# Performance work log

Hardware: AMD Instinct MI355X
Metric: run time of the kernel (lower is better)

Reference implementation:

```python
import jax, jax.numpy as jnp
import numpy as np
from jax.ops import segment_sum

N_NODES = 100000

def gcn_conv(x, ei, W, b, n):
    # PyG GCNConv: add self-loops, symmetric deg^-1/2 normalization,
    # linear transform (no lin bias), scatter-sum at target, then conv bias.
    src = jnp.concatenate([ei[0], jnp.arange(n)])  # [E+N]
    dst = jnp.concatenate([ei[1], jnp.arange(n)])
    deg = segment_sum(jnp.ones_like(dst, dtype=x.dtype), dst, num_segments=n)
    dinv = jnp.where(deg > 0, jax.lax.rsqrt(deg), 0.0)
    norm = dinv[src] * dinv[dst]                   # [E+N]
    h = x @ W.T                                    # [N, out] transform before gather
    msg = h[src] * norm[:, None]                   # [E+N, out]
    return segment_sum(msg, dst, num_segments=n) + b

def sage_conv_mean(x, ei, Wl, bl, Wr, n):
    # PyG SAGEConv(aggr='mean'): out = lin_l(mean_{j->i} x_j) + lin_r(x_i)
    src, dst = ei[0], ei[1]
    s = segment_sum(x[src], dst, num_segments=n)   # [N, d]
    cnt = segment_sum(jnp.ones_like(dst, dtype=x.dtype), dst, num_segments=n)
    mean = s / jnp.maximum(cnt, 1.0)[:, None]
    return mean @ Wl.T + bl + x @ Wr.T

def setup_inputs() -> dict:
    key = jax.random.key(0)
    k1, k2, k3, k4, k5, k6 = jax.random.split(key, 6)
    in_dim, hid = 128, 128
    n, e = N_NODES, 1600000
    feat = jax.random.normal(k1, (n, in_dim), dtype=jnp.float32)
    ei = jax.random.randint(k2, (2, e), 0, n, dtype=jnp.int64)
    W1 = jax.random.normal(k3, (hid, in_dim), dtype=jnp.float32) * 0.05
    b1 = jnp.zeros((hid,), dtype=jnp.float32)
    Wl = jax.random.normal(k4, (hid, hid), dtype=jnp.float32) * 0.05
    bl = jnp.zeros((hid,), dtype=jnp.float32)
    Wr = jax.random.normal(k5, (hid, hid), dtype=jnp.float32) * 0.05
    return {"feat": feat, "ei": ei, "W1": W1, "b1": b1, "Wl": Wl, "bl": bl, "Wr": Wr}

def reference(feat, ei, W1, b1, Wl, bl, Wr):
    n = feat.shape[0]
    h = jax.nn.relu(gcn_conv(feat, ei, W1, b1, n))
    h = jax.nn.relu(sage_conv_mean(h, ei, Wl, bl, Wr, n))
    return h
```

## Files before the change

### kernel.cpp

```cpp
#include <hip/hip_runtime.h>

typedef unsigned int uint;
typedef unsigned short ushort;
typedef short sv8 __attribute__((ext_vector_type(8)));
typedef float f32x4 __attribute__((ext_vector_type(4)));
typedef ushort u16x8 __attribute__((ext_vector_type(8)));

__device__ __forceinline__ ushort f2b(float f) {
  uint u = __float_as_uint(f);
  return (ushort)((u + 0x7FFFu + ((u >> 16) & 1u)) >> 16);
}
__device__ __forceinline__ float b2f_lo(uint p) { return __uint_as_float(p << 16); }
__device__ __forceinline__ float b2f_hi(uint p) { return __uint_as_float(p & 0xFFFF0000u); }
__device__ __forceinline__ uint cvtpk(float lo, float hi) {
  uint r;
  asm("v_cvt_pk_bf16_f32 %0, %1, %2" : "=v"(r) : "v"(lo), "v"(hi));
  return r;
}

#define MFMA16(acc, a, b) \
  asm volatile("v_mfma_f32_16x16x32_bf16 %0, %1, %2, %0" : "+v"(acc) : "v"(a), "v"(b))
#define DOT2(acc, p, d) \
  asm("v_dot2_f32_bf16 %0, %1, %2, %0" : "+v"(acc) : "v"(p), "v"(d))

#define GATHER16(SRC, jj)                                                     \
  {                                                                           \
    uint pa = (uint)__shfl((int)packed, (jj) + q);                            \
    uint pb = (uint)__shfl((int)packed, (jj) + 4 + q);                        \
    uint pc = (uint)__shfl((int)packed, (jj) + 8 + q);                        \
    uint pd = (uint)__shfl((int)packed, (jj) + 12 + q);                       \
    uint4 va = *(const uint4*)&SRC[(size_t)(pa & 0x1FFFFu) * 128 + lc * 8];   \
    uint4 vb = *(const uint4*)&SRC[(size_t)(pb & 0x1FFFFu) * 128 + lc * 8];   \
    uint4 vc = *(const uint4*)&SRC[(size_t)(pc & 0x1FFFFu) * 128 + lc * 8];   \
    uint4 vd = *(const uint4*)&SRC[(size_t)(pd & 0x1FFFFu) * 128 + lc * 8];   \
    uint dab = (pa >> 17) | ((pb >> 17) << 16);                               \
    uint dcd = (pc >> 17) | ((pd >> 17) << 16);                               \
    uint p;                                                                   \
    p = __builtin_amdgcn_perm(va.x, vb.x, 0x01000504u); DOT2(acc[0], p, dab); \
    p = __builtin_amdgcn_perm(va.x, vb.x, 0x03020706u); DOT2(acc[1], p, dab); \
    p = __builtin_amdgcn_perm(va.y, vb.y, 0x01000504u); DOT2(acc[2], p, dab); \
    p = __builtin_amdgcn_perm(va.y, vb.y, 0x03020706u); DOT2(acc[3], p, dab); \
    p = __builtin_amdgcn_perm(va.z, vb.z, 0x01000504u); DOT2(acc[4], p, dab); \
    p = __builtin_amdgcn_perm(va.z, vb.z, 0x03020706u); DOT2(acc[5], p, dab); \
    p = __builtin_amdgcn_perm(va.w, vb.w, 0x01000504u); DOT2(acc[6], p, dab); \
    p = __builtin_amdgcn_perm(va.w, vb.w, 0x03020706u); DOT2(acc[7], p, dab); \
    p = __builtin_amdgcn_perm(vc.x, vd.x, 0x01000504u); DOT2(acc[0], p, dcd); \
    p = __builtin_amdgcn_perm(vc.x, vd.x, 0x03020706u); DOT2(acc[1], p, dcd); \
    p = __builtin_amdgcn_perm(vc.y, vd.y, 0x01000504u); DOT2(acc[2], p, dcd); \
    p = __builtin_amdgcn_perm(vc.y, vd.y, 0x03020706u); DOT2(acc[3], p, dcd); \
    p = __builtin_amdgcn_perm(vc.z, vd.z, 0x01000504u); DOT2(acc[4], p, dcd); \
    p = __builtin_amdgcn_perm(vc.z, vd.z, 0x03020706u); DOT2(acc[5], p, dcd); \
    p = __builtin_amdgcn_perm(vc.w, vd.w, 0x01000504u); DOT2(acc[6], p, dcd); \
    p = __builtin_amdgcn_perm(vc.w, vd.w, 0x03020706u); DOT2(acc[7], p, dcd); \
  }


__global__ __launch_bounds__(256) void k_bhist(const int* __restrict__ dst,
                                               int* __restrict__ bhist, int E) {
  __shared__ int h[256];
  int t = threadIdx.x;
  h[t] = 0;
  __syncthreads();
#pragma unroll
  for (int i = 0; i < 16; ++i) {
    int idx = blockIdx.x * 16384 + i * 1024 + t * 4;
    if (idx + 4 <= E) {
      int4 d = *(const int4*)&dst[idx];
      atomicAdd(&h[d.x >> 10], 1);
      atomicAdd(&h[d.y >> 10], 1);
      atomicAdd(&h[d.z >> 10], 1);
      atomicAdd(&h[d.w >> 10], 1);
    } else {
      for (int k = 0; k < 4; ++k)
        if (idx + k < E) atomicAdd(&h[dst[idx + k] >> 10], 1);
    }
  }
  __syncthreads();
  if (h[t] > 0) atomicAdd(&bhist[t], h[t]);
}

__global__ __launch_bounds__(256) void k_bscan(const int* __restrict__ bhist,
                                               int* __restrict__ bbase,
                                               int* __restrict__ bcursor,
                                               int* __restrict__ rowptr,
                                               int NB, int N, int E) {
  __shared__ int s[256];
  int t = threadIdx.x;
  int v = (t < NB) ? bhist[t] : 0;
  s[t] = v;
  __syncthreads();
  for (int off = 1; off < 256; off <<= 1) {
    int u = (t >= off) ? s[t - off] : 0;
    __syncthreads();
    s[t] += u;
    __syncthreads();
  }
  if (t < NB) {
    bbase[t] = s[t] - v;
    bcursor[t] = s[t] - v;
  }
  if (t == 0) rowptr[N] = E;
}

__global__ __launch_bounds__(256) void k_scatter(const int* __restrict__ ei,
                                                 int* __restrict__ bcursor,
                                                 uint* __restrict__ keyval, int E) {
  __shared__ int h[256];
  __shared__ int base[256];
  int t = threadIdx.x;
  h[t] = 0;
  __syncthreads();
#pragma unroll
  for (int i = 0; i < 16; ++i) {
    int idx = blockIdx.x * 16384 + i * 1024 + t * 4;
    if (idx + 4 <= E) {
      int4 d = *(const int4*)&ei[E + idx];
      atomicAdd(&h[d.x >> 10], 1);
      atomicAdd(&h[d.y >> 10], 1);
      atomicAdd(&h[d.z >> 10], 1);
      atomicAdd(&h[d.w >> 10], 1);
    } else {
      for (int k = 0; k < 4; ++k)
        if (idx + k < E) atomicAdd(&h[ei[E + idx + k] >> 10], 1);
    }
  }
  __syncthreads();
  int hv = h[t];
  base[t] = (hv > 0) ? atomicAdd(&bcursor[t], hv) : 0;
  __syncthreads();
  h[t] = 0;
  __syncthreads();
#pragma unroll
  for (int i = 0; i < 16; ++i) {
    int idx = blockIdx.x * 16384 + i * 1024 + t * 4;
    if (idx + 4 <= E) {
      int4 sv = *(const int4*)&ei[idx];
      int4 dv = *(const int4*)&ei[E + idx];
      int b0 = dv.x >> 10, b1 = dv.y >> 10, b2 = dv.z >> 10, b3 = dv.w >> 10;
      int r0 = atomicAdd(&h[b0], 1);
      keyval[base[b0] + r0] = (uint)sv.x | (((uint)dv.x & 1023u) << 17);
      int r1 = atomicAdd(&h[b1], 1);
      keyval[base[b1] + r1] = (uint)sv.y | (((uint)dv.y & 1023u) << 17);
      int r2 = atomicAdd(&h[b2], 1);
      keyval[base[b2] + r2] = (uint)sv.z | (((uint)dv.z & 1023u) << 17);
      int r3 = atomicAdd(&h[b3], 1);
      keyval[base[b3] + r3] = (uint)sv.w | (((uint)dv.w & 1023u) << 17);
    } else {
      for (int k = 0; k < 4; ++k)
        if (idx + k < E) {
          int sv = ei[idx + k], dv = ei[E + idx + k];
          int b = dv >> 10;
          int r = atomicAdd(&h[b], 1);
          keyval[base[b] + r] = (uint)sv | (((uint)dv & 1023u) << 17);
        }
    }
  }
}

__global__ __launch_bounds__(1024) void k_build(const uint* __restrict__ keyval,
                                                const int* __restrict__ bbase,
                                                const int* __restrict__ bhist,
                                                int* __restrict__ rowptr,
                                                float* __restrict__ dinv,
                                                ushort* __restrict__ dinvb,
                                                int* __restrict__ col, int N) {
  __shared__ int c[1024];
  int b = blockIdx.x, t = threadIdx.x;
  int ebase = bbase[b], ecnt = bhist[b];
  int node0 = b << 10;
  c[t] = 0;
  __syncthreads();
  for (int i = t; i < ecnt; i += 1024)
    atomicAdd(&c[keyval[ebase + i] >> 17], 1);
  __syncthreads();
  int v = c[t];
  for (int off = 1; off < 1024; off <<= 1) {
    int u = (t >= off) ? c[t - off] : 0;
    __syncthreads();
    c[t] += u;
    __syncthreads();
  }
  int excl = c[t] - v;
  int node = node0 + t;
  if (node < N) {
    float dv = rsqrtf((float)(v + 1));
    rowptr[node] = ebase + excl;
    dinv[node] = dv;
    dinvb[node] = f2b(dv);
  }
  __syncthreads();
  c[t] = excl;
  __syncthreads();
  for (int i = t; i < ecnt; i += 1024) {
    uint kv = keyval[ebase + i];
    int r = atomicAdd(&c[kv >> 17], 1);
    col[ebase + r] = (int)(kv & 0x1FFFFu);
  }
}


__global__ __launch_bounds__(256) void k_gemm1(const float* __restrict__ A,
                                               const float* __restrict__ W,
                                               ushort* __restrict__ Hb, int N) {
  __shared__ __align__(16) ushort smem[17408];
  int t = threadIdx.x;
#pragma unroll
  for (int i = 0; i < 8; ++i) {
    int c_ = t + i * 256;
    int row = c_ >> 4, slot = c_ & 15;
    const float* wp = &W[row * 128 + slot * 8];
    float4 w0 = *(const float4*)wp;
    float4 w1 = *(const float4*)(wp + 4);
    uint4 v = make_uint4(cvtpk(w0.x, w0.y), cvtpk(w0.z, w0.w),
                         cvtpk(w1.x, w1.y), cvtpk(w1.z, w1.w));
    *(uint4*)&smem[row * 128 + ((slot ^ (row & 7)) << 3)] = v;
  }
  __syncthreads();

  int wv = t >> 6, l = t & 63;
  int lr = l & 15, lk = l >> 4;
  int r0 = blockIdx.x * 128 + wv * 32;
  f32x4 acc[2][8];
#pragma unroll
  for (int rb = 0; rb < 2; ++rb)
#pragma unroll
    for (int ct = 0; ct < 8; ++ct) acc[rb][ct] = (f32x4){0.f, 0.f, 0.f, 0.f};

#pragma unroll
  for (int kk = 0; kk < 4; ++kk) {
    sv8 af[2];
#pragma unroll
    for (int rb = 0; rb < 2; ++rb) {
      int r = r0 + rb * 16 + lr;
      if (r >= N) r = N - 1;
      const float* ap = &A[(size_t)r * 128 + kk * 32 + lk * 8];
      float4 a0 = *(const float4*)ap;
      float4 a1 = *(const float4*)(ap + 4);
      uint4 au = make_uint4(cvtpk(a0.x, a0.y), cvtpk(a0.z, a0.w),
                            cvtpk(a1.x, a1.y), cvtpk(a1.z, a1.w));
      af[rb] = *(sv8*)&au;
    }
#pragma unroll
    for (int ct = 0; ct < 8; ++ct) {
      int brow = ct * 16 + lr;
      sv8 bf = *(const sv8*)&smem[brow * 128 + (((kk * 4 + lk) ^ (brow & 7)) << 3)];
      MFMA16(acc[0][ct], af[0], bf);
      MFMA16(acc[1][ct], af[1], bf);
    }
  }
  asm volatile("s_nop 7\n\ts_nop 7");
  __syncthreads();
  ushort* ep = smem + wv * (32 * 136);
#pragma unroll
  for (int rb = 0; rb < 2; ++rb)
#pragma unroll
    for (int ct = 0; ct < 8; ++ct)
#pragma unroll
      for (int i = 0; i < 4; ++i)
        ep[(rb * 16 + lk * 4 + i) * 136 + ct * 16 + lr] = f2b(acc[rb][ct][i]);
#pragma unroll
  for (int it = 0; it < 4; ++it) {
    int row = it * 8 + (l >> 3);
    int gr = r0 + row;
    if (gr < N) {
#pragma unroll
      for (int cc = 0; cc < 2; ++cc) {
        int colv = cc * 64 + (l & 7) * 8;
        *(u16x8*)&Hb[(size_t)gr * 128 + colv] = *(const u16x8*)&ep[row * 136 + colv];
      }
    }
  }
}


__global__ __launch_bounds__(256) void k_gemm2(const ushort* __restrict__ Mb,
                                               const ushort* __restrict__ X1b,
                                               const float* __restrict__ Wl,
                                               const float* __restrict__ Wr,
                                               const float* __restrict__ bl,
                                               float* __restrict__ Out, int N) {
  __shared__ __align__(16) ushort smem[2 * 128 * 128];
  int t = threadIdx.x;
#pragma unroll
  for (int i = 0; i < 8; ++i) {
    int c_ = t + i * 256;
    int row = c_ >> 4, slot = c_ & 15;
    int off = (slot ^ (row & 7)) << 3;
    {
      const float* wp = &Wl[row * 128 + slot * 8];
      float4 w0 = *(const float4*)wp;
      float4 w1 = *(const float4*)(wp + 4);
      *(uint4*)&smem[row * 128 + off] =
          make_uint4(cvtpk(w0.x, w0.y), cvtpk(w0.z, w0.w),
                     cvtpk(w1.x, w1.y), cvtpk(w1.z, w1.w));
    }
    {
      const float* wp = &Wr[row * 128 + slot * 8];
      float4 w0 = *(const float4*)wp;
      float4 w1 = *(const float4*)(wp + 4);
      *(uint4*)&smem[16384 + row * 128 + off] =
          make_uint4(cvtpk(w0.x, w0.y), cvtpk(w0.z, w0.w),
                     cvtpk(w1.x, w1.y), cvtpk(w1.z, w1.w));
    }
  }
  __syncthreads();

  int wv = t >> 6, l = t & 63;
  int lr = l & 15, lk = l >> 4;
  int r0 = blockIdx.x * 128 + wv * 32;
  f32x4 acc[2][8];
#pragma unroll
  for (int rb = 0; rb < 2; ++rb)
#pragma unroll
    for (int ct = 0; ct < 8; ++ct) acc[rb][ct] = (f32x4){0.f, 0.f, 0.f, 0.f};

#pragma unroll
  for (int ph = 0; ph < 2; ++ph) {
    const ushort* Ab = ph ? X1b : Mb;
    const ushort* Wp = smem + ph * 16384;
#pragma unroll
    for (int kk = 0; kk < 4; ++kk) {
      sv8 af[2];
#pragma unroll
      for (int rb = 0; rb < 2; ++rb) {
        int r = r0 + rb * 16 + lr;
        if (r >= N) r = N - 1;
        af[rb] = *(const sv8*)&Ab[(size_t)r * 128 + kk * 32 + lk * 8];
      }
#pragma unroll
      for (int ct = 0; ct < 8; ++ct) {
        int brow = ct * 16 + lr;
        sv8 bf = *(const sv8*)&Wp[brow * 128 + (((kk * 4 + lk) ^ (brow & 7)) << 3)];
        MFMA16(acc[0][ct], af[0], bf);
        MFMA16(acc[1][ct], af[1], bf);
      }
    }
  }
  asm volatile("s_nop 7\n\ts_nop 7");
  __syncthreads();
  float* epf = (float*)smem + wv * (16 * 132);
#pragma unroll
  for (int rb = 0; rb < 2; ++rb) {
#pragma unroll
    for (int ct = 0; ct < 8; ++ct) {
      float bb = bl[ct * 16 + lr];
#pragma unroll
      for (int i = 0; i < 4; ++i)
        epf[(lk * 4 + i) * 132 + ct * 16 + lr] = fmaxf(acc[rb][ct][i] + bb, 0.f);
    }
#pragma unroll
    for (int it = 0; it < 2; ++it) {
      int row = it * 8 + (l >> 3);
      int gr = r0 + rb * 16 + row;
      if (gr < N) {
#pragma unroll
        for (int cc = 0; cc < 4; ++cc) {
          int colv = cc * 32 + (l & 7) * 4;
          *(float4*)&Out[(size_t)gr * 128 + colv] = *(const float4*)&epf[row * 132 + colv];
        }
      }
    }
  }
}


__global__ __launch_bounds__(256) void k_agg_gcn(const ushort* __restrict__ Hb,
                                                 const int* __restrict__ rowptr,
                                                 const int* __restrict__ col,
                                                 const float* __restrict__ dinv,
                                                 const ushort* __restrict__ dinvb,
                                                 const float* __restrict__ bias,
                                                 ushort* __restrict__ X1b, int N) {
  int wid = (blockIdx.x * 256 + threadIdx.x) >> 6;
  int l = threadIdx.x & 63;
  if (wid >= N) return;
  int q = l >> 4, lc = l & 15;
  float di = dinv[wid];
  float acc[8] = {0.f, 0.f, 0.f, 0.f, 0.f, 0.f, 0.f, 0.f};
  int s0 = rowptr[wid], s1 = rowptr[wid + 1];
  for (int j0 = s0; j0 < s1; j0 += 64) {
    int rem = s1 - j0;
    uint packed = 0;
    if (l < rem) {
      int ix = col[j0 + l];
      packed = (uint)ix | ((uint)dinvb[ix] << 17);
    }
    int m = rem < 64 ? rem : 64;
    for (int jj = 0; jj < m; jj += 16) GATHER16(Hb, jj);
  }
#pragma unroll
  for (int k = 0; k < 8; ++k) {
    acc[k] += __shfl_xor(acc[k], 16);
    acc[k] += __shfl_xor(acc[k], 32);
  }
  if (q == 0) {
    uint4 hv = *(const uint4*)&Hb[(size_t)wid * 128 + lc * 8];
    float4 b0 = *(const float4*)&bias[lc * 8];
    float4 b1 = *(const float4*)&bias[lc * 8 + 4];
    float hvf[8] = {b2f_lo(hv.x), b2f_hi(hv.x), b2f_lo(hv.y), b2f_hi(hv.y),
                    b2f_lo(hv.z), b2f_hi(hv.z), b2f_lo(hv.w), b2f_hi(hv.w)};
    float bb[8] = {b0.x, b0.y, b0.z, b0.w, b1.x, b1.y, b1.z, b1.w};
    float o[8];
#pragma unroll
    for (int k = 0; k < 8; ++k)
      o[k] = fmaxf((acc[k] + hvf[k] * di) * di + bb[k], 0.f);
    uint4 r = make_uint4(cvtpk(o[0], o[1]), cvtpk(o[2], o[3]),
                         cvtpk(o[4], o[5]), cvtpk(o[6], o[7]));
    *(uint4*)&X1b[(size_t)wid * 128 + lc * 8] = r;
  }
}

__global__ __launch_bounds__(256) void k_agg_mean(const ushort* __restrict__ Xb,
                                                  const int* __restrict__ rowptr,
                                                  const int* __restrict__ col,
                                                  ushort* __restrict__ Mb, int N) {
  int wid = (blockIdx.x * 256 + threadIdx.x) >> 6;
  int l = threadIdx.x & 63;
  if (wid >= N) return;
  int q = l >> 4, lc = l & 15;
  float acc[8] = {0.f, 0.f, 0.f, 0.f, 0.f, 0.f, 0.f, 0.f};
  int s0 = rowptr[wid], s1 = rowptr[wid + 1];
  for (int j0 = s0; j0 < s1; j0 += 64) {
    int rem = s1 - j0;
    uint packed = 0;
    if (l < rem) packed = (uint)col[j0 + l] | (0x3F80u << 17);
    int m = rem < 64 ? rem : 64;
    for (int jj = 0; jj < m; jj += 16) GATHER16(Xb, jj);
  }
#pragma unroll
  for (int k = 0; k < 8; ++k) {
    acc[k] += __shfl_xor(acc[k], 16);
    acc[k] += __shfl_xor(acc[k], 32);
  }
  if (q == 0) {
    int deg = s1 - s0;
    float inv = 1.f / (float)(deg > 0 ? deg : 1);
    uint4 r = make_uint4(cvtpk(acc[0] * inv, acc[1] * inv),
                         cvtpk(acc[2] * inv, acc[3] * inv),
                         cvtpk(acc[4] * inv, acc[5] * inv),
                         cvtpk(acc[6] * inv, acc[7] * inv));
    *(uint4*)&Mb[(size_t)wid * 128 + lc * 8] = r;
  }
}


extern "C" void kernel_launch(void* const* d_in, const int* in_sizes, int n_in,
                              void* d_out, int out_size, void* d_ws, size_t ws_size,
                              hipStream_t stream) {
  const float* feat = (const float*)d_in[0];
  const int* ei     = (const int*)d_in[1];
  const float* W1   = (const float*)d_in[2];
  const float* b1   = (const float*)d_in[3];
  const float* Wl   = (const float*)d_in[4];
  const float* bl   = (const float*)d_in[5];
  const float* Wr   = (const float*)d_in[6];
  float* out = (float*)d_out;

  int N = in_sizes[0] / 128;
  int E = in_sizes[1] / 2;

  char* ws = (char*)d_ws;
  size_t off = 0;
  auto alloc = [&](size_t bytes) {
    void* p = ws + off;
    off += (bytes + 255) & ~(size_t)255;
    return p;
  };
  ushort* Hb    = (ushort*)alloc((size_t)N * 128 * 2);
  ushort* X1b   = (ushort*)alloc((size_t)N * 128 * 2);
  int*   rowptr = (int*)alloc((size_t)(N + 1) * 4);
  float* dinv   = (float*)alloc((size_t)N * 4);
  ushort* dinvb = (ushort*)alloc((size_t)N * 2);
  int*   col    = (int*)alloc((size_t)E * 4);
  int*   bhist  = (int*)alloc(1024);
  int*   bbase  = (int*)alloc(1024);
  int*   bcursor= (int*)alloc(1024);
  uint* keyval = (uint*)Hb;

  int NB = (N + 1023) >> 10;
  int NBLK = (E + 16383) / 16384;

  hipMemsetAsync(bhist, 0, 1024, stream);
  k_bhist<<<NBLK, 256, 0, stream>>>(ei + E, bhist, E);
  k_bscan<<<1, 256, 0, stream>>>(bhist, bbase, bcursor, rowptr, NB, N, E);
  k_scatter<<<NBLK, 256, 0, stream>>>(ei, bcursor, keyval, E);
  k_build<<<NB, 1024, 0, stream>>>(keyval, bbase, bhist, rowptr, dinv, dinvb, col, N);

  int gb = (N + 127) / 128;
  k_gemm1<<<gb, 256, 0, stream>>>(feat, W1, Hb, N);
  k_agg_gcn<<<(N + 3) / 4, 256, 0, stream>>>(Hb, rowptr, col, dinv, dinvb, b1, X1b, N);
  k_agg_mean<<<(N + 3) / 4, 256, 0, stream>>>(X1b, rowptr, col, Hb, N);
  k_gemm2<<<gb, 256, 0, stream>>>(Hb, X1b, Wl, Wr, bl, out, N);
}
```

Baseline: 213.4 us.

## Replace atomic bucket cursors with per-block count scan; double GEMM row tile

The CSR build now writes per-block bucket histograms and runs a column-wise scan to give each block deterministic scatter offsets. This removes the second histogram pass in k_scatter, the global atomic cursors and the memset. Both GEMM kernels now handle 256 rows per block (64 per wave) instead of 128, which reuses each shared-memory weight fragment across four MFMAs. The cost is higher register pressure from 128 accumulator floats per lane, fewer blocks, and a serial single-block scan over 98 histogram rows.

```diff
diff --git a/kernel.cpp b/kernel.cpp
--- a/kernel.cpp
+++ b/kernel.cpp
@@ -55,8 +55,8 @@
   }
 
 
-__global__ __launch_bounds__(256) void k_bhist(const int* __restrict__ dst,
-                                               int* __restrict__ bhist, int E) {
+__global__ __launch_bounds__(256) void k_hist1(const int* __restrict__ dst,
+                                               int* __restrict__ counts, int E) {
   __shared__ int h[256];
   int t = threadIdx.x;
   h[t] = 0;
@@ -76,58 +76,46 @@
     }
   }
   __syncthreads();
-  if (h[t] > 0) atomicAdd(&bhist[t], h[t]);
-}
-
-__global__ __launch_bounds__(256) void k_bscan(const int* __restrict__ bhist,
-                                               int* __restrict__ bbase,
-                                               int* __restrict__ bcursor,
-                                               int* __restrict__ rowptr,
-                                               int NB, int N, int E) {
+  counts[blockIdx.x * 256 + t] = h[t];
+}
+
+__global__ __launch_bounds__(256) void k_colscan(int* __restrict__ counts,
+                                                 int* __restrict__ bbase,
+                                                 int* __restrict__ btot,
+                                                 int* __restrict__ rowptr,
+                                                 int NBLK, int N, int E) {
   __shared__ int s[256];
-  int t = threadIdx.x;
-  int v = (t < NB) ? bhist[t] : 0;
-  s[t] = v;
-  __syncthreads();
+  int b = threadIdx.x;
+  int run = 0;
+#pragma unroll 4
+  for (int blk = 0; blk < NBLK; ++blk) {
+    int v = counts[blk * 256 + b];
+    counts[blk * 256 + b] = run;
+    run += v;
+  }
+  s[b] = run;
+  __syncthreads();
+  int incl = run;
   for (int off = 1; off < 256; off <<= 1) {
-    int u = (t >= off) ? s[t - off] : 0;
+    int u = (b >= off) ? s[b - off] : 0;
     __syncthreads();
-    s[t] += u;
+    s[b] += u;
     __syncthreads();
   }
-  if (t < NB) {
-    bbase[t] = s[t] - v;
-    bcursor[t] = s[t] - v;
-  }
-  if (t == 0) rowptr[N] = E;
+  incl = s[b];
+  bbase[b] = incl - run;
+  btot[b] = run;
+  if (b == 0) rowptr[N] = E;
 }
 
 __global__ __launch_bounds__(256) void k_scatter(const int* __restrict__ ei,
-                                                 int* __restrict__ bcursor,
+                                                 const int* __restrict__ counts,
+                                                 const int* __restrict__ bbase,
                                                  uint* __restrict__ keyval, int E) {
   __shared__ int h[256];
   __shared__ int base[256];
   int t = threadIdx.x;
-  h[t] = 0;
-  __syncthreads();
-#pragma unroll
-  for (int i = 0; i < 16; ++i) {
-    int idx = blockIdx.x * 16384 + i * 1024 + t * 4;
-    if (idx + 4 <= E) {
-      int4 d = *(const int4*)&ei[E + idx];
-      atomicAdd(&h[d.x >> 10], 1);
-      atomicAdd(&h[d.y >> 10], 1);
-      atomicAdd(&h[d.z >> 10], 1);
-      atomicAdd(&h[d.w >> 10], 1);
-    } else {
-      for (int k = 0; k < 4; ++k)
-        if (idx + k < E) atomicAdd(&h[ei[E + idx + k] >> 10], 1);
-    }
-  }
-  __syncthreads();
-  int hv = h[t];
-  base[t] = (hv > 0) ? atomicAdd(&bcursor[t], hv) : 0;
-  __syncthreads();
+  base[t] = bbase[t] + counts[blockIdx.x * 256 + t];
   h[t] = 0;
   __syncthreads();
 #pragma unroll
@@ -159,14 +147,14 @@
 
 __global__ __launch_bounds__(1024) void k_build(const uint* __restrict__ keyval,
                                                 const int* __restrict__ bbase,
-                                                const int* __restrict__ bhist,
+                                                const int* __restrict__ btot,
                                                 int* __restrict__ rowptr,
                                                 float* __restrict__ dinv,
                                                 ushort* __restrict__ dinvb,
                                                 int* __restrict__ col, int N) {
   __shared__ int c[1024];
   int b = blockIdx.x, t = threadIdx.x;
-  int ebase = bbase[b], ecnt = bhist[b];
+  int ebase = bbase[b], ecnt = btot[b];
   int node0 = b << 10;
   c[t] = 0;
   __syncthreads();
@@ -219,18 +207,18 @@
 
   int wv = t >> 6, l = t & 63;
   int lr = l & 15, lk = l >> 4;
-  int r0 = blockIdx.x * 128 + wv * 32;
-  f32x4 acc[2][8];
-#pragma unroll
-  for (int rb = 0; rb < 2; ++rb)
+  int r0 = blockIdx.x * 256 + wv * 64;
+  f32x4 acc[4][8];
+#pragma unroll
+  for (int rb = 0; rb < 4; ++rb)
 #pragma unroll
     for (int ct = 0; ct < 8; ++ct) acc[rb][ct] = (f32x4){0.f, 0.f, 0.f, 0.f};
 
 #pragma unroll
   for (int kk = 0; kk < 4; ++kk) {
-    sv8 af[2];
-#pragma unroll
-    for (int rb = 0; rb < 2; ++rb) {
+    sv8 af[4];
+#pragma unroll
+    for (int rb = 0; rb < 4; ++rb) {
       int r = r0 + rb * 16 + lr;
       if (r >= N) r = N - 1;
       const float* ap = &A[(size_t)r * 128 + kk * 32 + lk * 8];
@@ -246,27 +234,30 @@
       sv8 bf = *(const sv8*)&smem[brow * 128 + (((kk * 4 + lk) ^ (brow & 7)) << 3)];
       MFMA16(acc[0][ct], af[0], bf);
       MFMA16(acc[1][ct], af[1], bf);
+      MFMA16(acc[2][ct], af[2], bf);
+      MFMA16(acc[3][ct], af[3], bf);
     }
   }
   asm volatile("s_nop 7\n\ts_nop 7");
   __syncthreads();
-  ushort* ep = smem + wv * (32 * 136);
-#pragma unroll
-  for (int rb = 0; rb < 2; ++rb)
+  ushort* ep = smem + wv * (16 * 136);
+#pragma unroll
+  for (int rb = 0; rb < 4; ++rb) {
 #pragma unroll
     for (int ct = 0; ct < 8; ++ct)
 #pragma unroll
       for (int i = 0; i < 4; ++i)
-        ep[(rb * 16 + lk * 4 + i) * 136 + ct * 16 + lr] = f2b(acc[rb][ct][i]);
-#pragma unroll
-  for (int it = 0; it < 4; ++it) {
-    int row = it * 8 + (l >> 3);
-    int gr = r0 + row;
-    if (gr < N) {
-#pragma unroll
-      for (int cc = 0; cc < 2; ++cc) {
-        int colv = cc * 64 + (l & 7) * 8;
-        *(u16x8*)&Hb[(size_t)gr * 128 + colv] = *(const u16x8*)&ep[row * 136 + colv];
+        ep[(lk * 4 + i) * 136 + ct * 16 + lr] = f2b(acc[rb][ct][i]);
+#pragma unroll
+    for (int it = 0; it < 2; ++it) {
+      int row = it * 8 + (l >> 3);
+      int gr = r0 + rb * 16 + row;
+      if (gr < N) {
+#pragma unroll
+        for (int cc = 0; cc < 2; ++cc) {
+          int colv = cc * 64 + (l & 7) * 8;
+          *(u16x8*)&Hb[(size_t)gr * 128 + colv] = *(const u16x8*)&ep[row * 136 + colv];
+        }
       }
     }
   }
@@ -307,10 +298,10 @@
 
   int wv = t >> 6, l = t & 63;
   int lr = l & 15, lk = l >> 4;
-  int r0 = blockIdx.x * 128 + wv * 32;
-  f32x4 acc[2][8];
-#pragma unroll
-  for (int rb = 0; rb < 2; ++rb)
+  int r0 = blockIdx.x * 256 + wv * 64;
+  f32x4 acc[4][8];
+#pragma unroll
+  for (int rb = 0; rb < 4; ++rb)
 #pragma unroll
     for (int ct = 0; ct < 8; ++ct) acc[rb][ct] = (f32x4){0.f, 0.f, 0.f, 0.f};
 
@@ -320,9 +311,9 @@
     const ushort* Wp = smem + ph * 16384;
 #pragma unroll
     for (int kk = 0; kk < 4; ++kk) {
-      sv8 af[2];
-#pragma unroll
-      for (int rb = 0; rb < 2; ++rb) {
+      sv8 af[4];
+#pragma unroll
+      for (int rb = 0; rb < 4; ++rb) {
         int r = r0 + rb * 16 + lr;
         if (r >= N) r = N - 1;
         af[rb] = *(const sv8*)&Ab[(size_t)r * 128 + kk * 32 + lk * 8];
@@ -333,21 +324,24 @@
         sv8 bf = *(const sv8*)&Wp[brow * 128 + (((kk * 4 + lk) ^ (brow & 7)) << 3)];
         MFMA16(acc[0][ct], af[0], bf);
         MFMA16(acc[1][ct], af[1], bf);
+        MFMA16(acc[2][ct], af[2], bf);
+        MFMA16(acc[3][ct], af[3], bf);
       }
     }
   }
   asm volatile("s_nop 7\n\ts_nop 7");
   __syncthreads();
   float* epf = (float*)smem + wv * (16 * 132);
-#pragma unroll
-  for (int rb = 0; rb < 2; ++rb) {
-#pragma unroll
-    for (int ct = 0; ct < 8; ++ct) {
-      float bb = bl[ct * 16 + lr];
+  float bb[8];
+#pragma unroll
+  for (int ct = 0; ct < 8; ++ct) bb[ct] = bl[ct * 16 + lr];
+#pragma unroll
+  for (int rb = 0; rb < 4; ++rb) {
+#pragma unroll
+    for (int ct = 0; ct < 8; ++ct)
 #pragma unroll
       for (int i = 0; i < 4; ++i)
-        epf[(lk * 4 + i) * 132 + ct * 16 + lr] = fmaxf(acc[rb][ct][i] + bb, 0.f);
-    }
+        epf[(lk * 4 + i) * 132 + ct * 16 + lr] = fmaxf(acc[rb][ct][i] + bb[ct], 0.f);
 #pragma unroll
     for (int it = 0; it < 2; ++it) {
       int row = it * 8 + (l >> 3);
@@ -472,21 +466,20 @@
   float* dinv   = (float*)alloc((size_t)N * 4);
   ushort* dinvb = (ushort*)alloc((size_t)N * 2);
   int*   col    = (int*)alloc((size_t)E * 4);
-  int*   bhist  = (int*)alloc(1024);
+  int*   counts = (int*)alloc(128 * 256 * 4);
   int*   bbase  = (int*)alloc(1024);
-  int*   bcursor= (int*)alloc(1024);
+  int*   btot   = (int*)alloc(1024);
   uint* keyval = (uint*)Hb;
 
   int NB = (N + 1023) >> 10;
   int NBLK = (E + 16383) / 16384;
 
-  hipMemsetAsync(bhist, 0, 1024, stream);
-  k_bhist<<<NBLK, 256, 0, stream>>>(ei + E, bhist, E);
-  k_bscan<<<1, 256, 0, stream>>>(bhist, bbase, bcursor, rowptr, NB, N, E);
-  k_scatter<<<NBLK, 256, 0, stream>>>(ei, bcursor, keyval, E);
-  k_build<<<NB, 1024, 0, stream>>>(keyval, bbase, bhist, rowptr, dinv, dinvb, col, N);
-
-  int gb = (N + 127) / 128;
+  k_hist1<<<NBLK, 256, 0, stream>>>(ei + E, counts, E);
+  k_colscan<<<1, 256, 0, stream>>>(counts, bbase, btot, rowptr, NBLK, N, E);
+  k_scatter<<<NBLK, 256, 0, stream>>>(ei, counts, bbase, keyval, E);
+  k_build<<<NB, 1024, 0, stream>>>(keyval, bbase, btot, rowptr, dinv, dinvb, col, N);
+
+  int gb = (N + 255) / 256;
   k_gemm1<<<gb, 256, 0, stream>>>(feat, W1, Hb, N);
   k_agg_gcn<<<(N + 3) / 4, 256, 0, stream>>>(Hb, rowptr, col, dinv, dinvb, b1, X1b, N);
   k_agg_mean<<<(N + 3) / 4, 256, 0, stream>>>(X1b, rowptr, col, Hb, N);
```

After: 206.9 us. -3.0%, faster.
